# Kernel optimization log

Hardware: AMD Instinct MI355X
Metric: run time of the kernel (lower is better)

The kernel has to match this reference:

```python
import jax, jax.numpy as jnp
import numpy as np

ROW = COL = 8   # unfold tile size
KS = 5          # gaussian raster kernel size
C1 = 6          # high-freq feature split

def conv2d(x, w, b=None, pad=0):
    y = jax.lax.conv_general_dilated(x, w, (1, 1), [(pad, pad), (pad, pad)],
                                     dimension_numbers=('NCHW', 'OIHW', 'NCHW'))
    if b is not None:
        y = y + b[None, :, None, None]
    return y

def unfold_tiles(x, r, c):
    # non-overlapping Unfold(kernel=(r,c), stride=(r,c)) -> [B*L, C, r, c]
    B, C, H, W = x.shape
    x = x.reshape(B, C, H // r, r, W // c, c).transpose(0, 2, 4, 1, 3, 5)
    return x.reshape(B * (H // r) * (W // c), C, r, c)

def fold_tiles(t, B, C, H, W, r, c):
    t = t.reshape(B, H // r, W // c, C, r, c).transpose(0, 3, 1, 4, 2, 5)
    return t.reshape(B, C, H, W)

def setup_inputs() -> dict:
    key = jax.random.key(0)
    ks = jax.random.split(key, 16)
    B, NF, H, W, P = 32, 48, 128, 128, 81
    inp = {
        'ms': jax.random.normal(ks[0], (B, 4, 32, 32), jnp.float32),
        'feat': jax.random.normal(ks[1], (B, NF, H, W), jnp.float32),
        'V': jax.random.normal(ks[2], (B, NF, H, W), jnp.float32),
        'logits_raw': jax.random.normal(ks[3], (B, P, H, W), jnp.float32),
        'sigma_x': jax.random.uniform(ks[4], (P,), jnp.float32, 0.2, 3.0),
        'sigma_y': jax.random.uniform(ks[5], (P,), jnp.float32, 0.2, 3.0),
        'opacity': jax.random.uniform(ks[6], (P,), jnp.float32, 0.1, 1.0),
        'rho': jax.random.uniform(ks[7], (P,), jnp.float32, -0.9, 0.9),
        'w_v2': jax.random.normal(ks[8], (42, 42, 1, 1), jnp.float32) * 0.05,
        'w_fine': jax.random.normal(ks[9], (4, NF, 3, 3), jnp.float32) * 0.05,
        'b_fine': jax.random.normal(ks[10], (4,), jnp.float32) * 0.05,
        'w_res': jax.random.normal(ks[11], (4, NF, 1, 1), jnp.float32) * 0.05,
        'b_res': jax.random.normal(ks[12], (4,), jnp.float32) * 0.05,
    }
    return inp

def reference(ms, feat, V, logits_raw, sigma_x, sigma_y, opacity, rho,
              w_v2, w_fine, b_fine, w_res, b_res):
    B, nf, H, W = feat.shape
    # soft class assignment (gumbel_softmax tau=1, zero-noise deterministic surrogate)
    logits = jax.nn.softmax(logits_raw, axis=1)
    feat1, lr_feat = feat[:, :C1], feat[:, C1:]
    V1, V2 = V[:, :C1], V[:, C1:]
    # H,W are already multiples of ROW/COL -> bicubic-to-same-size is identity
    uf = unfold_tiles(feat1, ROW, COL)        # [B*L, c1, 8, 8]
    ul = unfold_tiles(logits, ROW, COL)       # [B*L, P, 8, 8]
    uv1 = unfold_tiles(V1, ROW, COL)          # [B*L, c1, 8, 8]
    # weighted gaussian params per in-tile position, averaged over all tiles
    pm = ul.reshape(ul.shape[0], ul.shape[1], -1).mean(axis=0)   # [P, 64]
    wsx = sigma_x @ pm; wsy = sigma_y @ pm                       # [64]
    wop = opacity @ pm; wr = rho @ pm                            # [64]
    # 2x2 covariance per point, analytic inverse
    a = wsx ** 2; bcv = wr * wsx * wsy; d = wsy ** 2
    det = a * d - bcv ** 2
    i00 = d / det; i01 = -bcv / det; i11 = a / det
    ax = jnp.linspace(-5.0, 5.0, KS)
    xx = ax[:, None]; yy = ax[None, :]
    z = -0.5 * (i00[:, None, None] * xx ** 2 + 2.0 * i01[:, None, None] * xx * yy
                + i11[:, None, None] * yy ** 2)
    kern = jnp.exp(z) / (2.0 * jnp.pi * jnp.sqrt(det))[:, None, None]   # [64, KS, KS]
    kern = kern / kern.max(axis=(-2, -1), keepdims=True)
    kern = kern * wop[:, None, None]
    # splat: place each point's kernel centered at its grid position in the 8x8 tile
    pad = KS // 2
    ii = jnp.arange(ROW * COL) // COL
    jj = jnp.arange(ROW * COL) % COL
    canvas = jnp.zeros((ROW + 2 * pad, COL + 2 * pad), kern.dtype)
    place = jax.vmap(lambda k, i, j: jax.lax.dynamic_update_slice(canvas, k, (i, j)))
    K = place(kern, ii, jj)[:, pad:pad + ROW, pad:pad + COL]             # [64, 8, 8]
    colors = uf.reshape(uf.shape[0], C1, ROW * COL)                      # [N, c1, 64]
    rendered = jnp.einsum('ncp,phw->nchw', colors, K) * uv1              # modulate by V1
    hr = fold_tiles(rendered, B, C1, H, W, ROW, COL)                     # [B, c1, H, W]
    # squeeze-style channel attention on low branch, modulated by V2
    gap = lr_feat.mean(axis=(2, 3), keepdims=True)
    attn = jax.nn.sigmoid(conv2d(gap, w_v2))
    lr_mod = lr_feat * attn * V2
    out_feat = jnp.concatenate([hr, lr_mod], axis=1)                     # [B, n_feats, H, W]
    up_ms = jax.image.resize(ms, (B, ms.shape[1], H, W), method='bilinear')
    out = conv2d(out_feat, w_fine, b_fine, pad=1) + conv2d(feat, w_res, b_res) + up_ms
    return out
```

## Files before the change

### kernel.cpp

```cpp
#include <hip/hip_runtime.h>

#define NBATCH 32
#define NFEAT 48
#define C1c 6
#define LRC 42
#define HH 128
#define WW 128
#define HWSZ 16384
#define NP 81
#define NQ 64

#define OFF_PM   0
#define OFF_GAP  5184
#define OFF_K    6528
#define OFF_ATTN 10624
#define OFF_WB   11968
#define OFF_HR   14272

__global__ __launch_bounds__(256, 2) void k_softmax_pm(const float* __restrict__ logits,
                                                       float* __restrict__ pm_sum) {
    int bid = blockIdx.x;
    int b   = bid >> 4;
    int ygp = (bid >> 2) & 3;
    int qq  = bid & 3;
    int tid = threadIdx.x;
    int x   = tid & 127;
    int yg  = ygp * 2 + (tid >> 7);

    float acc[NP];
#pragma unroll
    for (int p = 0; p < NP; ++p) acc[p] = 0.f;

    for (int k = 0; k < 4; ++k) {
        int y = yg + 8 * (qq * 4 + k);
        const float* base = logits + (size_t)b * NP * HWSZ + (y << 7) + x;
        float ev[NP];
        float s = 0.f;
#pragma unroll
        for (int p = 0; p < NP; ++p) { ev[p] = __expf(base[(size_t)p * HWSZ]); s += ev[p]; }
        float inv = 1.f / s;
#pragma unroll
        for (int p = 0; p < NP; ++p) acc[p] += ev[p] * inv;
    }
    int lane = tid & 63;
#pragma unroll
    for (int p = 0; p < NP; ++p) {
        float e = acc[p];
        e += __shfl_xor(e, 8);
        e += __shfl_xor(e, 16);
        e += __shfl_xor(e, 32);
        if (lane < 8) atomicAdd(&pm_sum[p * NQ + (yg << 3) + lane], e);
    }
}

__global__ __launch_bounds__(256) void k_gap(const float* __restrict__ feat,
                                             float* __restrict__ gap) {
    int bid = blockIdx.x;
    int b = bid / LRC, c = bid % LRC;
    const float4* p = (const float4*)(feat + ((size_t)b * NFEAT + C1c + c) * HWSZ);
    float s = 0.f;
    for (int i = threadIdx.x; i < HWSZ / 4; i += 256) {
        float4 v = p[i];
        s += (v.x + v.y) + (v.z + v.w);
    }
    s += __shfl_xor(s, 1);  s += __shfl_xor(s, 2);  s += __shfl_xor(s, 4);
    s += __shfl_xor(s, 8);  s += __shfl_xor(s, 16); s += __shfl_xor(s, 32);
    __shared__ float w4[4];
    if ((threadIdx.x & 63) == 0) w4[threadIdx.x >> 6] = s;
    __syncthreads();
    if (threadIdx.x == 0) gap[bid] = w4[0] + w4[1] + w4[2] + w4[3];
}

__global__ __launch_bounds__(256) void k_small(const float* __restrict__ pm_sum,
                                               const float* __restrict__ gap_sum,
                                               const float* __restrict__ sigx,
                                               const float* __restrict__ sigy,
                                               const float* __restrict__ opac,
                                               const float* __restrict__ rho,
                                               const float* __restrict__ w_v2,
                                               const float* __restrict__ w_fine,
                                               const float* __restrict__ w_res,
                                               float* __restrict__ Kmat,
                                               float* __restrict__ attn,
                                               float* __restrict__ wbuf) {
    int tid = threadIdx.x;
    if (tid < 64) {
        int q = tid;
        float wsx = 0.f, wsy = 0.f, wop = 0.f, wr = 0.f;
        for (int p = 0; p < NP; ++p) {
            float pv = pm_sum[p * NQ + q] * (1.f / 8192.f);
            wsx += sigx[p] * pv;
            wsy += sigy[p] * pv;
            wop += opac[p] * pv;
            wr  += rho[p]  * pv;
        }
        float a = wsx * wsx, d = wsy * wsy, bc = wr * wsx * wsy;
        float det = a * d - bc * bc;
        float i00 = d / det, i01 = -bc / det, i11 = a / det;
        int iq = q >> 3, jq = q & 7;
        for (int h = 0; h < 8; ++h)
            for (int w = 0; w < 8; ++w) {
                int ki = h - iq + 2, kj = w - jq + 2;
                float val = 0.f;
                if (ki >= 0 && ki < 5 && kj >= 0 && kj < 5) {
                    float xx = -5.f + 2.5f * ki, yy = -5.f + 2.5f * kj;
                    val = wop * __expf(-0.5f * (i00 * xx * xx + 2.f * i01 * xx * yy + i11 * yy * yy));
                }
                Kmat[(q << 6) + (h << 3) + w] = val;
            }
    }
    for (int i = tid; i < NBATCH * LRC; i += 256) {
        int b = i / LRC, co = i % LRC;
        float s = 0.f;
        for (int ci = 0; ci < LRC; ++ci) s += w_v2[co * LRC + ci] * gap_sum[b * LRC + ci];
        s *= (1.f / 16384.f);
        attn[i] = 1.f / (1.f + __expf(-s));
    }
    for (int i = tid; i < NFEAT * 48; i += 256) {
        int c = i / 48, j = i - c * 48;
        float v = 0.f;
        if (j < 36) v = w_fine[(j / 9) * (NFEAT * 9) + c * 9 + (j % 9)];
        else if (j < 40) v = w_res[(j - 36) * NFEAT + c];
        wbuf[i] = v;
    }
}

__global__ __launch_bounds__(256) void k_hr(const float* __restrict__ feat,
                                            const float* __restrict__ V,
                                            const float* __restrict__ Kmat,
                                            float* __restrict__ hr) {
    __shared__ __align__(16) float lds[16384];
    float* lK = lds;
    float* lF = lds + 4096;
    int bid = blockIdx.x;
    int b = bid >> 3;
    int y0 = (bid & 7) << 4;
    int tid = threadIdx.x;
    for (int i = tid; i < 4096; i += 256) lK[i] = Kmat[i];
    for (int i = tid; i < 12288; i += 256) {
        int c = i >> 11, rem = i & 2047;
        lF[i] = feat[(((size_t)b * NFEAT + c) << 14) + (((size_t)y0 + (rem >> 7)) << 7) + (rem & 127)];
    }
    __syncthreads();
    int tile = tid >> 3, hrow = tid & 7;
    int tr = tile >> 4, tx = tile & 15;
    float acc[6][8];
#pragma unroll
    for (int c = 0; c < 6; ++c)
#pragma unroll
        for (int j = 0; j < 8; ++j) acc[c][j] = 0.f;
    int fbase = (tr << 3) * 128 + (tx << 3);
    for (int q = 0; q < 64; ++q) {
        int iq = q >> 3, jq = q & 7;
        const float4 k0 = *(const float4*)&lK[(q << 6) + (hrow << 3)];
        const float4 k1 = *(const float4*)&lK[(q << 6) + (hrow << 3) + 4];
#pragma unroll
        for (int c = 0; c < 6; ++c) {
            float col = lF[(c << 11) + fbase + (iq << 7) + jq];
            acc[c][0] += col * k0.x; acc[c][1] += col * k0.y;
            acc[c][2] += col * k0.z; acc[c][3] += col * k0.w;
            acc[c][4] += col * k1.x; acc[c][5] += col * k1.y;
            acc[c][6] += col * k1.z; acc[c][7] += col * k1.w;
        }
    }
    int y = y0 + (tr << 3) + hrow;
#pragma unroll
    for (int c = 0; c < 6; ++c) {
        const float4* vp = (const float4*)(V + (((size_t)b * NFEAT + c) << 14) + ((size_t)y << 7) + (tx << 3));
        float4 v0 = vp[0], v1 = vp[1];
        float4 r0, r1;
        r0.x = acc[c][0] * v0.x; r0.y = acc[c][1] * v0.y; r0.z = acc[c][2] * v0.z; r0.w = acc[c][3] * v0.w;
        r1.x = acc[c][4] * v1.x; r1.y = acc[c][5] * v1.y; r1.z = acc[c][6] * v1.z; r1.w = acc[c][7] * v1.w;
        float4* op = (float4*)(hr + (((size_t)b * C1c + c) << 14) + ((size_t)y << 7) + (tx << 3));
        op[0] = r0; op[1] = r1;
    }
}

#define CCH 8
__global__ __launch_bounds__(256, 4) void k_conv(const float* __restrict__ feat,
                                                 const float* __restrict__ V,
                                                 const float* __restrict__ ms,
                                                 const float* __restrict__ wbuf,
                                                 const float* __restrict__ b_fine,
                                                 const float* __restrict__ b_res,
                                                 const float* __restrict__ hr,
                                                 const float* __restrict__ attn,
                                                 float* __restrict__ out) {
    __shared__ __align__(16) float s_in[CCH][18 * 36];
    int bid = blockIdx.x;
    int b   = bid >> 5;
    int t32 = bid & 31;
    int ty0 = (t32 >> 2) << 4;
    int tx0 = (t32 & 3) << 5;
    int tid = threadIdx.x;
    int ty  = tid >> 5;
    int lx  = tid & 31;
    int py  = ty0 + 2 * ty;
    int gx  = tx0 + lx;

    float a[4][2];
#pragma unroll
    for (int o = 0; o < 4; ++o) { a[o][0] = 0.f; a[o][1] = 0.f; }

    for (int cb = 0; cb < NFEAT; cb += CCH) {
        __syncthreads();
        for (int cc = 0; cc < CCH; ++cc) {
            int c = cb + cc;
            if (c < C1c) {
                const float* src = hr + (((size_t)b * C1c + c) << 14);
                for (int i = tid; i < 612; i += 256) {
                    int r = i / 34, cl = i - r * 34;
                    int sy = ty0 - 1 + r, sx = tx0 - 1 + cl;
                    float v = 0.f;
                    if (sy >= 0 && sy < HH && sx >= 0 && sx < WW) v = src[(sy << 7) + sx];
                    s_in[cc][r * 36 + cl] = v;
                }
            } else {
                float am = attn[b * LRC + (c - C1c)];
                const float* fsrc = feat + (((size_t)b * NFEAT + c) << 14);
                const float* vsrc = V    + (((size_t)b * NFEAT + c) << 14);
                for (int i = tid; i < 612; i += 256) {
                    int r = i / 34, cl = i - r * 34;
                    int sy = ty0 - 1 + r, sx = tx0 - 1 + cl;
                    float v = 0.f;
                    if (sy >= 0 && sy < HH && sx >= 0 && sx < WW) {
                        int g = (sy << 7) + sx;
                        v = fsrc[g] * am * vsrc[g];
                    }
                    s_in[cc][r * 36 + cl] = v;
                }
            }
        }
        __syncthreads();
        for (int cc = 0; cc < CCH; ++cc) {
            int c = cb + cc;
            const float* wc = wbuf + c * 48;
            float4 s0 = *(const float4*)&s_in[cc][(2 * ty + 0) * 36 + lx];
            float4 s1 = *(const float4*)&s_in[cc][(2 * ty + 1) * 36 + lx];
            float4 s2 = *(const float4*)&s_in[cc][(2 * ty + 2) * 36 + lx];
            float4 s3 = *(const float4*)&s_in[cc][(2 * ty + 3) * 36 + lx];
            const float* fc = feat + (((size_t)b * NFEAT + c) << 14);
            float fc0 = fc[(py << 7) + gx];
            float fc1 = fc[((py + 1) << 7) + gx];
#pragma unroll
            for (int o = 0; o < 4; ++o) {
                float w00 = wc[o * 9 + 0], w01 = wc[o * 9 + 1], w02 = wc[o * 9 + 2];
                float w10 = wc[o * 9 + 3], w11 = wc[o * 9 + 4], w12 = wc[o * 9 + 5];
                float w20 = wc[o * 9 + 6], w21 = wc[o * 9 + 7], w22 = wc[o * 9 + 8];
                float wr  = wc[36 + o];
                float r0 = w00 * s0.x + w01 * s0.y + w02 * s0.z
                         + w10 * s1.x + w11 * s1.y + w12 * s1.z
                         + w20 * s2.x + w21 * s2.y + w22 * s2.z
                         + wr * fc0;
                float r1 = w00 * s1.x + w01 * s1.y + w02 * s1.z
                         + w10 * s2.x + w11 * s2.y + w12 * s2.z
                         + w20 * s3.x + w21 * s3.y + w22 * s3.z
                         + wr * fc1;
                a[o][0] += r0;
                a[o][1] += r1;
            }
        }
    }
#pragma unroll
    for (int o = 0; o < 4; ++o) {
        const float* mb = ms + ((size_t)(b * 4 + o) << 10);
        float addc = b_fine[o] + b_res[o];
#pragma unroll
        for (int yy = 0; yy < 2; ++yy) {
            int gy = py + yy;
            float syf = (gy + 0.5f) * 0.25f - 0.5f;
            int y0i = (int)floorf(syf); float fy = syf - (float)y0i;
            int y0c = min(31, max(0, y0i)), y1c = min(31, max(0, y0i + 1));
            float sxf = (gx + 0.5f) * 0.25f - 0.5f;
            int x0i = (int)floorf(sxf); float fx = sxf - (float)x0i;
            int x0c = min(31, max(0, x0i)), x1c = min(31, max(0, x0i + 1));
            float m00 = mb[(y0c << 5) + x0c], m01 = mb[(y0c << 5) + x1c];
            float m10 = mb[(y1c << 5) + x0c], m11 = mb[(y1c << 5) + x1c];
            float up = (m00 * (1.f - fx) + m01 * fx) * (1.f - fy)
                     + (m10 * (1.f - fx) + m11 * fx) * fy;
            out[((size_t)(b * 4 + o) << 14) + (gy << 7) + gx] = a[o][yy] + addc + up;
        }
    }
}

extern "C" void kernel_launch(void* const* d_in, const int* in_sizes, int n_in,
                              void* d_out, int out_size, void* d_ws, size_t ws_size,
                              hipStream_t stream) {
    (void)in_sizes; (void)n_in; (void)out_size; (void)ws_size;
    const float* ms     = (const float*)d_in[0];
    const float* feat   = (const float*)d_in[1];
    const float* V      = (const float*)d_in[2];
    const float* logits = (const float*)d_in[3];
    const float* sigx   = (const float*)d_in[4];
    const float* sigy   = (const float*)d_in[5];
    const float* opac   = (const float*)d_in[6];
    const float* rho    = (const float*)d_in[7];
    const float* w_v2   = (const float*)d_in[8];
    const float* w_fine = (const float*)d_in[9];
    const float* b_fine = (const float*)d_in[10];
    const float* w_res  = (const float*)d_in[11];
    const float* b_res  = (const float*)d_in[12];
    float* ws  = (float*)d_ws;
    float* out = (float*)d_out;

    hipMemsetAsync(ws + OFF_PM, 0, (size_t)NP * NQ * sizeof(float), stream);
    k_softmax_pm<<<512, 256, 0, stream>>>(logits, ws + OFF_PM);
    k_gap<<<NBATCH * LRC, 256, 0, stream>>>(feat, ws + OFF_GAP);
    k_small<<<1, 256, 0, stream>>>(ws + OFF_PM, ws + OFF_GAP, sigx, sigy, opac, rho, w_v2,
                                   w_fine, w_res, ws + OFF_K, ws + OFF_ATTN, ws + OFF_WB);
    k_hr<<<256, 256, 0, stream>>>(feat, V, ws + OFF_K, ws + OFF_HR);
    k_conv<<<1024, 256, 0, stream>>>(feat, V, ms, ws + OFF_WB, b_fine, b_res,
                                     ws + OFF_HR, ws + OFF_ATTN, out);
}
```

Before: 220.9 us.

## Merge softmax and GAP kernels, split hr channels, restructure conv to one pixel per thread

The softmax/probability-map kernel and the global-average-pool kernel become a single launch, with block index deciding which job a block does, so the two independent reductions run concurrently. k_hr splits its six channels across two blocks, doubling the grid and halving LDS use. It also pads the kernel matrix in LDS to cut bank conflicts. k_conv moves to 512 threads with one output pixel per thread and loads the halo tile with precomputed offsets and masks. The 1x1 residual conv is accumulated during the tile load and exchanged through LDS, trading extra LDS and a sync for fewer redundant global reads of feat.

```diff
diff --git a/kernel.cpp b/kernel.cpp
--- a/kernel.cpp
+++ b/kernel.cpp
@@ -17,58 +17,57 @@
 #define OFF_WB   11968
 #define OFF_HR   14272
 
-__global__ __launch_bounds__(256, 2) void k_softmax_pm(const float* __restrict__ logits,
-                                                       float* __restrict__ pm_sum) {
+__global__ __launch_bounds__(256, 2) void k_phase1(const float* __restrict__ logits,
+                                                   const float* __restrict__ feat,
+                                                   float* __restrict__ pm_sum,
+                                                   float* __restrict__ gap) {
     int bid = blockIdx.x;
-    int b   = bid >> 4;
-    int ygp = (bid >> 2) & 3;
-    int qq  = bid & 3;
     int tid = threadIdx.x;
-    int x   = tid & 127;
-    int yg  = ygp * 2 + (tid >> 7);
-
-    float acc[NP];
-#pragma unroll
-    for (int p = 0; p < NP; ++p) acc[p] = 0.f;
-
-    for (int k = 0; k < 4; ++k) {
-        int y = yg + 8 * (qq * 4 + k);
-        const float* base = logits + (size_t)b * NP * HWSZ + (y << 7) + x;
-        float ev[NP];
+    if (bid < 512) {
+        int b   = bid >> 4;
+        int ygp = (bid >> 2) & 3;
+        int qq  = bid & 3;
+        int x   = tid & 127;
+        int yg  = ygp * 2 + (tid >> 7);
+        float acc[NP];
+#pragma unroll
+        for (int p = 0; p < NP; ++p) acc[p] = 0.f;
+        for (int k = 0; k < 4; ++k) {
+            int y = yg + 8 * (qq * 4 + k);
+            const float* base = logits + (size_t)b * NP * HWSZ + (y << 7) + x;
+            float ev[NP];
+            float s = 0.f;
+#pragma unroll
+            for (int p = 0; p < NP; ++p) { ev[p] = __expf(base[(size_t)p * HWSZ]); s += ev[p]; }
+            float inv = 1.f / s;
+#pragma unroll
+            for (int p = 0; p < NP; ++p) acc[p] += ev[p] * inv;
+        }
+        int lane = tid & 63;
+#pragma unroll
+        for (int p = 0; p < NP; ++p) {
+            float e = acc[p];
+            e += __shfl_xor(e, 8);
+            e += __shfl_xor(e, 16);
+            e += __shfl_xor(e, 32);
+            if (lane < 8) atomicAdd(&pm_sum[p * NQ + (yg << 3) + lane], e);
+        }
+    } else {
+        int gid = bid - 512;
+        int b = gid / LRC, c = gid % LRC;
+        const float4* p4 = (const float4*)(feat + ((size_t)b * NFEAT + C1c + c) * HWSZ);
         float s = 0.f;
-#pragma unroll
-        for (int p = 0; p < NP; ++p) { ev[p] = __expf(base[(size_t)p * HWSZ]); s += ev[p]; }
-        float inv = 1.f / s;
-#pragma unroll
-        for (int p = 0; p < NP; ++p) acc[p] += ev[p] * inv;
-    }
-    int lane = tid & 63;
-#pragma unroll
-    for (int p = 0; p < NP; ++p) {
-        float e = acc[p];
-        e += __shfl_xor(e, 8);
-        e += __shfl_xor(e, 16);
-        e += __shfl_xor(e, 32);
-        if (lane < 8) atomicAdd(&pm_sum[p * NQ + (yg << 3) + lane], e);
-    }
-}
-
-__global__ __launch_bounds__(256) void k_gap(const float* __restrict__ feat,
-                                             float* __restrict__ gap) {
-    int bid = blockIdx.x;
-    int b = bid / LRC, c = bid % LRC;
-    const float4* p = (const float4*)(feat + ((size_t)b * NFEAT + C1c + c) * HWSZ);
-    float s = 0.f;
-    for (int i = threadIdx.x; i < HWSZ / 4; i += 256) {
-        float4 v = p[i];
-        s += (v.x + v.y) + (v.z + v.w);
-    }
-    s += __shfl_xor(s, 1);  s += __shfl_xor(s, 2);  s += __shfl_xor(s, 4);
-    s += __shfl_xor(s, 8);  s += __shfl_xor(s, 16); s += __shfl_xor(s, 32);
-    __shared__ float w4[4];
-    if ((threadIdx.x & 63) == 0) w4[threadIdx.x >> 6] = s;
-    __syncthreads();
-    if (threadIdx.x == 0) gap[bid] = w4[0] + w4[1] + w4[2] + w4[3];
+        for (int i = tid; i < HWSZ / 4; i += 256) {
+            float4 v = p4[i];
+            s += (v.x + v.y) + (v.z + v.w);
+        }
+        s += __shfl_xor(s, 1);  s += __shfl_xor(s, 2);  s += __shfl_xor(s, 4);
+        s += __shfl_xor(s, 8);  s += __shfl_xor(s, 16); s += __shfl_xor(s, 32);
+        __shared__ float w4[4];
+        if ((tid & 63) == 0) w4[tid >> 6] = s;
+        __syncthreads();
+        if (tid == 0) gap[gid] = w4[0] + w4[1] + w4[2] + w4[3];
+    }
 }
 
 __global__ __launch_bounds__(256) void k_small(const float* __restrict__ pm_sum,
@@ -129,33 +128,37 @@
                                             const float* __restrict__ V,
                                             const float* __restrict__ Kmat,
                                             float* __restrict__ hr) {
-    __shared__ __align__(16) float lds[16384];
-    float* lK = lds;
-    float* lF = lds + 4096;
-    int bid = blockIdx.x;
-    int b = bid >> 3;
-    int y0 = (bid & 7) << 4;
-    int tid = threadIdx.x;
-    for (int i = tid; i < 4096; i += 256) lK[i] = Kmat[i];
-    for (int i = tid; i < 12288; i += 256) {
+    __shared__ __align__(16) float lK[64 * 96];
+    __shared__ __align__(16) float lF[3 * 16 * 128];
+    int bid   = blockIdx.x;
+    int b     = bid >> 4;
+    int strip = (bid >> 1) & 7;
+    int ch    = (bid & 1) * 3;
+    int y0    = strip << 4;
+    int tid   = threadIdx.x;
+    for (int i = tid; i < 4096; i += 256) {
+        int q = i >> 6, hj = i & 63;
+        lK[q * 96 + (hj >> 3) * 12 + (hj & 7)] = Kmat[i];
+    }
+    for (int i = tid; i < 6144; i += 256) {
         int c = i >> 11, rem = i & 2047;
-        lF[i] = feat[(((size_t)b * NFEAT + c) << 14) + (((size_t)y0 + (rem >> 7)) << 7) + (rem & 127)];
+        lF[i] = feat[(((size_t)b * NFEAT + ch + c) << 14) + (((size_t)y0 + (rem >> 7)) << 7) + (rem & 127)];
     }
     __syncthreads();
     int tile = tid >> 3, hrow = tid & 7;
     int tr = tile >> 4, tx = tile & 15;
-    float acc[6][8];
-#pragma unroll
-    for (int c = 0; c < 6; ++c)
+    float acc[3][8];
+#pragma unroll
+    for (int c = 0; c < 3; ++c)
 #pragma unroll
         for (int j = 0; j < 8; ++j) acc[c][j] = 0.f;
     int fbase = (tr << 3) * 128 + (tx << 3);
     for (int q = 0; q < 64; ++q) {
         int iq = q >> 3, jq = q & 7;
-        const float4 k0 = *(const float4*)&lK[(q << 6) + (hrow << 3)];
-        const float4 k1 = *(const float4*)&lK[(q << 6) + (hrow << 3) + 4];
-#pragma unroll
-        for (int c = 0; c < 6; ++c) {
+        const float4 k0 = *(const float4*)&lK[q * 96 + hrow * 12];
+        const float4 k1 = *(const float4*)&lK[q * 96 + hrow * 12 + 4];
+#pragma unroll
+        for (int c = 0; c < 3; ++c) {
             float col = lF[(c << 11) + fbase + (iq << 7) + jq];
             acc[c][0] += col * k0.x; acc[c][1] += col * k0.y;
             acc[c][2] += col * k0.z; acc[c][3] += col * k0.w;
@@ -165,19 +168,19 @@
     }
     int y = y0 + (tr << 3) + hrow;
 #pragma unroll
-    for (int c = 0; c < 6; ++c) {
-        const float4* vp = (const float4*)(V + (((size_t)b * NFEAT + c) << 14) + ((size_t)y << 7) + (tx << 3));
+    for (int c = 0; c < 3; ++c) {
+        const float4* vp = (const float4*)(V + (((size_t)b * NFEAT + ch + c) << 14) + ((size_t)y << 7) + (tx << 3));
         float4 v0 = vp[0], v1 = vp[1];
         float4 r0, r1;
         r0.x = acc[c][0] * v0.x; r0.y = acc[c][1] * v0.y; r0.z = acc[c][2] * v0.z; r0.w = acc[c][3] * v0.w;
         r1.x = acc[c][4] * v1.x; r1.y = acc[c][5] * v1.y; r1.z = acc[c][6] * v1.z; r1.w = acc[c][7] * v1.w;
-        float4* op = (float4*)(hr + (((size_t)b * C1c + c) << 14) + ((size_t)y << 7) + (tx << 3));
+        float4* op = (float4*)(hr + (((size_t)b * C1c + ch + c) << 14) + ((size_t)y << 7) + (tx << 3));
         op[0] = r0; op[1] = r1;
     }
 }
 
 #define CCH 8
-__global__ __launch_bounds__(256, 4) void k_conv(const float* __restrict__ feat,
+__global__ __launch_bounds__(512, 6) void k_conv(const float* __restrict__ feat,
                                                  const float* __restrict__ V,
                                                  const float* __restrict__ ms,
                                                  const float* __restrict__ wbuf,
@@ -186,100 +189,119 @@
                                                  const float* __restrict__ hr,
                                                  const float* __restrict__ attn,
                                                  float* __restrict__ out) {
-    __shared__ __align__(16) float s_in[CCH][18 * 36];
+    __shared__ __align__(16) float s_in[CCH][648];
+    __shared__ __align__(16) float s_acc[4][512];
     int bid = blockIdx.x;
     int b   = bid >> 5;
     int t32 = bid & 31;
     int ty0 = (t32 >> 2) << 4;
     int tx0 = (t32 & 3) << 5;
     int tid = threadIdx.x;
-    int ty  = tid >> 5;
-    int lx  = tid & 31;
-    int py  = ty0 + 2 * ty;
-    int gx  = tx0 + lx;
-
-    float a[4][2];
-#pragma unroll
-    for (int o = 0; o < 4; ++o) { a[o][0] = 0.f; a[o][1] = 0.f; }
+    int ty  = tid >> 5, lx = tid & 31;
+    int gy  = ty0 + ty, gx = tx0 + lx;
+
+    int r0 = tid / 36, c0 = tid - r0 * 36;
+    int sy0 = ty0 - 1 + r0, sx0 = tx0 - 1 + c0;
+    float fm0 = (c0 < 34 && sy0 >= 0 && sy0 < HH && sx0 >= 0 && sx0 < WW) ? 1.f : 0.f;
+    int off0 = (min(HH - 1, max(0, sy0)) << 7) + min(WW - 1, max(0, sx0));
+    bool i0in = (r0 >= 1 && r0 <= 16 && c0 >= 1 && c0 <= 32);
+    float im0 = i0in ? 1.f : 0.f;
+    int pix0 = (r0 - 1) * 32 + (c0 - 1);
+
+    int i1 = tid + 512;
+    bool has1 = (i1 < 648);
+    int r1 = i1 / 36, c1 = i1 - r1 * 36;
+    int sy1 = ty0 - 1 + r1, sx1 = tx0 - 1 + c1;
+    float fm1 = (has1 && c1 < 34 && sy1 < HH && sx1 >= 0 && sx1 < WW) ? 1.f : 0.f;
+    int off1 = (min(HH - 1, sy1) << 7) + min(WW - 1, max(0, sx1));
+    bool i1in = (has1 && r1 >= 1 && r1 <= 16 && c1 >= 1 && c1 <= 32);
+    float im1 = i1in ? 1.f : 0.f;
+    int pix1 = (r1 - 1) * 32 + (c1 - 1);
+
+    float a0 = 0.f, a1 = 0.f, a2 = 0.f, a3 = 0.f;
+    float x10[4] = {0.f, 0.f, 0.f, 0.f};
+    float x11[4] = {0.f, 0.f, 0.f, 0.f};
 
     for (int cb = 0; cb < NFEAT; cb += CCH) {
         __syncthreads();
+#pragma unroll
         for (int cc = 0; cc < CCH; ++cc) {
             int c = cb + cc;
+            const float* wc = wbuf + c * 48;
+            const float* fsrc = feat + (((size_t)b * NFEAT + c) << 14);
+            float wr0 = wc[36], wr1 = wc[37], wr2 = wc[38], wr3 = wc[39];
             if (c < C1c) {
-                const float* src = hr + (((size_t)b * C1c + c) << 14);
-                for (int i = tid; i < 612; i += 256) {
-                    int r = i / 34, cl = i - r * 34;
-                    int sy = ty0 - 1 + r, sx = tx0 - 1 + cl;
-                    float v = 0.f;
-                    if (sy >= 0 && sy < HH && sx >= 0 && sx < WW) v = src[(sy << 7) + sx];
-                    s_in[cc][r * 36 + cl] = v;
+                const float* hsrc = hr + (((size_t)b * C1c + c) << 14);
+                float f0 = fsrc[off0], h0 = hsrc[off0];
+                s_in[cc][tid] = h0 * fm0;
+                float ff0 = f0 * im0;
+                x10[0] += wr0 * ff0; x10[1] += wr1 * ff0; x10[2] += wr2 * ff0; x10[3] += wr3 * ff0;
+                if (has1) {
+                    float f1 = fsrc[off1], h1 = hsrc[off1];
+                    s_in[cc][i1] = h1 * fm1;
+                    float ff1 = f1 * im1;
+                    x11[0] += wr0 * ff1; x11[1] += wr1 * ff1; x11[2] += wr2 * ff1; x11[3] += wr3 * ff1;
                 }
             } else {
                 float am = attn[b * LRC + (c - C1c)];
-                const float* fsrc = feat + (((size_t)b * NFEAT + c) << 14);
-                const float* vsrc = V    + (((size_t)b * NFEAT + c) << 14);
-                for (int i = tid; i < 612; i += 256) {
-                    int r = i / 34, cl = i - r * 34;
-                    int sy = ty0 - 1 + r, sx = tx0 - 1 + cl;
-                    float v = 0.f;
-                    if (sy >= 0 && sy < HH && sx >= 0 && sx < WW) {
-                        int g = (sy << 7) + sx;
-                        v = fsrc[g] * am * vsrc[g];
-                    }
-                    s_in[cc][r * 36 + cl] = v;
+                const float* vsrc = V + (((size_t)b * NFEAT + c) << 14);
+                float f0 = fsrc[off0], v0 = vsrc[off0];
+                s_in[cc][tid] = f0 * v0 * (am * fm0);
+                float ff0 = f0 * im0;
+                x10[0] += wr0 * ff0; x10[1] += wr1 * ff0; x10[2] += wr2 * ff0; x10[3] += wr3 * ff0;
+                if (has1) {
+                    float f1 = fsrc[off1], v1 = vsrc[off1];
+                    s_in[cc][i1] = f1 * v1 * (am * fm1);
+                    float ff1 = f1 * im1;
+                    x11[0] += wr0 * ff1; x11[1] += wr1 * ff1; x11[2] += wr2 * ff1; x11[3] += wr3 * ff1;
                 }
             }
         }
         __syncthreads();
+        int base = ty * 36 + lx;
+#pragma unroll
         for (int cc = 0; cc < CCH; ++cc) {
             int c = cb + cc;
             const float* wc = wbuf + c * 48;
-            float4 s0 = *(const float4*)&s_in[cc][(2 * ty + 0) * 36 + lx];
-            float4 s1 = *(const float4*)&s_in[cc][(2 * ty + 1) * 36 + lx];
-            float4 s2 = *(const float4*)&s_in[cc][(2 * ty + 2) * 36 + lx];
-            float4 s3 = *(const float4*)&s_in[cc][(2 * ty + 3) * 36 + lx];
-            const float* fc = feat + (((size_t)b * NFEAT + c) << 14);
-            float fc0 = fc[(py << 7) + gx];
-            float fc1 = fc[((py + 1) << 7) + gx];
-#pragma unroll
-            for (int o = 0; o < 4; ++o) {
-                float w00 = wc[o * 9 + 0], w01 = wc[o * 9 + 1], w02 = wc[o * 9 + 2];
-                float w10 = wc[o * 9 + 3], w11 = wc[o * 9 + 4], w12 = wc[o * 9 + 5];
-                float w20 = wc[o * 9 + 6], w21 = wc[o * 9 + 7], w22 = wc[o * 9 + 8];
-                float wr  = wc[36 + o];
-                float r0 = w00 * s0.x + w01 * s0.y + w02 * s0.z
-                         + w10 * s1.x + w11 * s1.y + w12 * s1.z
-                         + w20 * s2.x + w21 * s2.y + w22 * s2.z
-                         + wr * fc0;
-                float r1 = w00 * s1.x + w01 * s1.y + w02 * s1.z
-                         + w10 * s2.x + w11 * s2.y + w12 * s2.z
-                         + w20 * s3.x + w21 * s3.y + w22 * s3.z
-                         + wr * fc1;
-                a[o][0] += r0;
-                a[o][1] += r1;
-            }
-        }
-    }
+            const float* sp = &s_in[cc][base];
+            float t00 = sp[0],  t01 = sp[1],  t02 = sp[2];
+            float t10 = sp[36], t11 = sp[37], t12 = sp[38];
+            float t20 = sp[72], t21 = sp[73], t22 = sp[74];
+            a0 += wc[0] * t00 + wc[1] * t01 + wc[2] * t02
+                + wc[3] * t10 + wc[4] * t11 + wc[5] * t12
+                + wc[6] * t20 + wc[7] * t21 + wc[8] * t22;
+            a1 += wc[9]  * t00 + wc[10] * t01 + wc[11] * t02
+                + wc[12] * t10 + wc[13] * t11 + wc[14] * t12
+                + wc[15] * t20 + wc[16] * t21 + wc[17] * t22;
+            a2 += wc[18] * t00 + wc[19] * t01 + wc[20] * t02
+                + wc[21] * t10 + wc[22] * t11 + wc[23] * t12
+                + wc[24] * t20 + wc[25] * t21 + wc[26] * t22;
+            a3 += wc[27] * t00 + wc[28] * t01 + wc[29] * t02
+                + wc[30] * t10 + wc[31] * t11 + wc[32] * t12
+                + wc[33] * t20 + wc[34] * t21 + wc[35] * t22;
+        }
+    }
+    if (i0in) { s_acc[0][pix0] = x10[0]; s_acc[1][pix0] = x10[1]; s_acc[2][pix0] = x10[2]; s_acc[3][pix0] = x10[3]; }
+    if (i1in) { s_acc[0][pix1] = x11[0]; s_acc[1][pix1] = x11[1]; s_acc[2][pix1] = x11[2]; s_acc[3][pix1] = x11[3]; }
+    __syncthreads();
+    int pix = ty * 32 + lx;
+    float acc1x1[4] = { s_acc[0][pix], s_acc[1][pix], s_acc[2][pix], s_acc[3][pix] };
+    float av[4] = { a0, a1, a2, a3 };
+    float syf = (gy + 0.5f) * 0.25f - 0.5f;
+    int y0i = (int)floorf(syf); float fy = syf - (float)y0i;
+    int y0c = min(31, max(0, y0i)), y1c = min(31, max(0, y0i + 1));
+    float sxf = (gx + 0.5f) * 0.25f - 0.5f;
+    int x0i = (int)floorf(sxf); float fx = sxf - (float)x0i;
+    int x0c = min(31, max(0, x0i)), x1c = min(31, max(0, x0i + 1));
 #pragma unroll
     for (int o = 0; o < 4; ++o) {
         const float* mb = ms + ((size_t)(b * 4 + o) << 10);
-        float addc = b_fine[o] + b_res[o];
-#pragma unroll
-        for (int yy = 0; yy < 2; ++yy) {
-            int gy = py + yy;
-            float syf = (gy + 0.5f) * 0.25f - 0.5f;
-            int y0i = (int)floorf(syf); float fy = syf - (float)y0i;
-            int y0c = min(31, max(0, y0i)), y1c = min(31, max(0, y0i + 1));
-            float sxf = (gx + 0.5f) * 0.25f - 0.5f;
-            int x0i = (int)floorf(sxf); float fx = sxf - (float)x0i;
-            int x0c = min(31, max(0, x0i)), x1c = min(31, max(0, x0i + 1));
-            float m00 = mb[(y0c << 5) + x0c], m01 = mb[(y0c << 5) + x1c];
-            float m10 = mb[(y1c << 5) + x0c], m11 = mb[(y1c << 5) + x1c];
-            float up = (m00 * (1.f - fx) + m01 * fx) * (1.f - fy)
-                     + (m10 * (1.f - fx) + m11 * fx) * fy;
-            out[((size_t)(b * 4 + o) << 14) + (gy << 7) + gx] = a[o][yy] + addc + up;
-        }
+        float m00 = mb[(y0c << 5) + x0c], m01 = mb[(y0c << 5) + x1c];
+        float m10 = mb[(y1c << 5) + x0c], m11 = mb[(y1c << 5) + x1c];
+        float up = (m00 * (1.f - fx) + m01 * fx) * (1.f - fy)
+                 + (m10 * (1.f - fx) + m11 * fx) * fy;
+        out[((size_t)(b * 4 + o) << 14) + (gy << 7) + gx] =
+            av[o] + acc1x1[o] + b_fine[o] + b_res[o] + up;
     }
 }
 
@@ -304,11 +326,10 @@
     float* out = (float*)d_out;
 
     hipMemsetAsync(ws + OFF_PM, 0, (size_t)NP * NQ * sizeof(float), stream);
-    k_softmax_pm<<<512, 256, 0, stream>>>(logits, ws + OFF_PM);
-    k_gap<<<NBATCH * LRC, 256, 0, stream>>>(feat, ws + OFF_GAP);
+    k_phase1<<<512 + NBATCH * LRC, 256, 0, stream>>>(logits, feat, ws + OFF_PM, ws + OFF_GAP);
     k_small<<<1, 256, 0, stream>>>(ws + OFF_PM, ws + OFF_GAP, sigx, sigy, opac, rho, w_v2,
                                    w_fine, w_res, ws + OFF_K, ws + OFF_ATTN, ws + OFF_WB);
-    k_hr<<<256, 256, 0, stream>>>(feat, V, ws + OFF_K, ws + OFF_HR);
-    k_conv<<<1024, 256, 0, stream>>>(feat, V, ms, ws + OFF_WB, b_fine, b_res,
+    k_hr<<<512, 256, 0, stream>>>(feat, V, ws + OFF_K, ws + OFF_HR);
+    k_conv<<<1024, 512, 0, stream>>>(feat, V, ms, ws + OFF_WB, b_fine, b_res,
                                      ws + OFF_HR, ws + OFF_ATTN, out);
 }
```

New measurement: 289.6 us. +31.1%, slower.
